# Optimization experiments

Hardware: AMD Instinct MI355X
Metric: run time of the kernel (lower is better)

The kernel has to match this reference:

```python
import jax, jax.numpy as jnp
import numpy as np

B, D_IN, H, D_OUT = 4096, 4096, 2048, 1000
LN_EPS = 1e-5


def setup_inputs() -> dict:
    key = jax.random.key(0)
    ks = jax.random.split(key, 8)
    s_in = 1.0 / np.sqrt(H)  # torch RNN init: U(-1/sqrt(H), 1/sqrt(H))
    inp = {
        "x": jax.random.normal(ks[0], (B, D_IN), dtype=jnp.float32),
        "W_ih0": jax.random.uniform(ks[1], (H, D_IN), jnp.float32, -s_in, s_in),
        "b_ih0": jax.random.uniform(ks[2], (H,), jnp.float32, -s_in, s_in),
        "b_hh0": jax.random.uniform(ks[3], (H,), jnp.float32, -s_in, s_in),
        "W_ih1": jax.random.uniform(ks[4], (H, H), jnp.float32, -s_in, s_in),
        "b_ih1": jax.random.uniform(ks[5], (H,), jnp.float32, -s_in, s_in),
        "b_hh1": jax.random.uniform(ks[6], (H,), jnp.float32, -s_in, s_in),
        "ln_g": jnp.ones((2 * H,), jnp.float32),
        "ln_b": jnp.zeros((2 * H,), jnp.float32),
        "fc_W": jax.random.uniform(ks[7], (D_OUT, 2 * H), jnp.float32, -1.0 / np.sqrt(2 * H), 1.0 / np.sqrt(2 * H)),
        "fc_b": jnp.zeros((D_OUT,), jnp.float32),
    }
    return inp


def reference(x, W_ih0, b_ih0, b_hh0, W_ih1, b_ih1, b_hh1, ln_g, ln_b, fc_W, fc_b):
    # seq_len == 1, h0 == 0 -> W_hh terms vanish; only biases remain.
    h1 = jnp.tanh(x @ W_ih0.T + b_ih0 + b_hh0)          # [B, H]
    h2 = jnp.tanh(h1 @ W_ih1.T + b_ih1 + b_hh1)         # [B, H]
    # last_hidden == mean_pooled (single step) -> concat duplicates h2
    combined = jnp.concatenate([h2, h2], axis=1)        # [B, 2H]
    mu = combined.mean(axis=-1, keepdims=True)
    var = combined.var(axis=-1, keepdims=True)
    normed = (combined - mu) * jax.lax.rsqrt(var + LN_EPS) * ln_g + ln_b
    # dropout is identity in eval mode
    return normed @ fc_W.T + fc_b                        # [B, D_OUT]
```

## Files before the change

kernel.cpp:

```cpp
#include <hip/hip_runtime.h>
#include <hip/hip_bf16.h>

typedef __attribute__((ext_vector_type(8))) unsigned short ushort8;
typedef __attribute__((ext_vector_type(8))) __bf16 bf16x8;
typedef __attribute__((ext_vector_type(4))) float f32x4;
typedef __attribute__((ext_vector_type(4))) float floatx4;

__device__ __forceinline__ unsigned short f2bf(float f) {
    unsigned u = __builtin_bit_cast(unsigned, f);
    u += 0x7fffu + ((u >> 16) & 1u);
    return (unsigned short)(u >> 16);
}
__device__ __forceinline__ float bf2f(unsigned short h) {
    unsigned u = ((unsigned)h) << 16;
    return __builtin_bit_cast(float, u);
}

__device__ __forceinline__ void gload_lds16(const void* g, void* l) {
    __builtin_amdgcn_global_load_lds(
        (const __attribute__((address_space(1))) void*)g,
        (__attribute__((address_space(3))) void*)l,
        16, 0, 0);
}

#define BAR()      asm volatile("s_barrier" ::: "memory")
#define WAIT_VM6() asm volatile("s_waitcnt vmcnt(6)" ::: "memory")
#define WAIT_VM0() asm volatile("s_waitcnt vmcnt(0)" ::: "memory")

__global__ __launch_bounds__(256) void cvt_f2bf(const float* __restrict__ in,
                                                unsigned short* __restrict__ out,
                                                int n8) {
    int i = blockIdx.x * 256 + threadIdx.x;
    if (i >= n8) return;
    floatx4 a = ((const floatx4*)in)[2 * i];
    floatx4 b = ((const floatx4*)in)[2 * i + 1];
    ushort8 o;
#pragma unroll
    for (int j = 0; j < 4; ++j) { o[j] = f2bf(a[j]); o[4 + j] = f2bf(b[j]); }
    ((ushort8*)out)[i] = o;
}

__global__ __launch_bounds__(256) void weff_kernel(const float* __restrict__ fcW,
                                                   const float* __restrict__ lng,
                                                   const float* __restrict__ lnb,
                                                   const float* __restrict__ fcb,
                                                   unsigned short* __restrict__ weff,
                                                   float* __restrict__ cc) {
    int o = blockIdx.x;
    int tid = threadIdx.x;
    if (o >= 1000) {
        ushort8 z = {0, 0, 0, 0, 0, 0, 0, 0};
        ((ushort8*)(weff + (size_t)o * 2048))[tid] = z;
        if (tid == 0) cc[o] = 0.f;
        return;
    }
    const float* wrow = fcW + (size_t)o * 4096;
    int j0 = tid * 8;
    floatx4 wa  = *(const floatx4*)(wrow + j0);
    floatx4 wb  = *(const floatx4*)(wrow + j0 + 4);
    floatx4 wa2 = *(const floatx4*)(wrow + 2048 + j0);
    floatx4 wb2 = *(const floatx4*)(wrow + 2048 + j0 + 4);
    floatx4 ga  = *(const floatx4*)(lng + j0);
    floatx4 gb  = *(const floatx4*)(lng + j0 + 4);
    floatx4 ga2 = *(const floatx4*)(lng + 2048 + j0);
    floatx4 gb2 = *(const floatx4*)(lng + 2048 + j0 + 4);
    floatx4 ba  = *(const floatx4*)(lnb + j0);
    floatx4 bb  = *(const floatx4*)(lnb + j0 + 4);
    floatx4 ba2 = *(const floatx4*)(lnb + 2048 + j0);
    floatx4 bb2 = *(const floatx4*)(lnb + 2048 + j0 + 4);
    ushort8 o8;
    float acc = 0.f;
#pragma unroll
    for (int j = 0; j < 4; ++j) {
        o8[j] = f2bf(ga[j] * wa[j] + ga2[j] * wa2[j]);
        acc += ba[j] * wa[j] + ba2[j] * wa2[j];
        o8[4 + j] = f2bf(gb[j] * wb[j] + gb2[j] * wb2[j]);
        acc += bb[j] * wb[j] + bb2[j] * wb2[j];
    }
    ((ushort8*)(weff + (size_t)o * 2048))[tid] = o8;
#pragma unroll
    for (int d = 32; d; d >>= 1) acc += __shfl_down(acc, d);
    __shared__ float red[4];
    if ((tid & 63) == 0) red[tid >> 6] = acc;
    __syncthreads();
    if (tid == 0) cc[o] = fcb[o] + red[0] + red[1] + red[2] + red[3];
}

__global__ __launch_bounds__(256) void ln_kernel(const unsigned short* __restrict__ h2,
                                                 unsigned short* __restrict__ z) {
    int row = blockIdx.x, tid = threadIdx.x;
    ushort8 v = ((const ushort8*)(h2 + (size_t)row * 2048))[tid];
    float f[8];
    float s = 0.f, s2 = 0.f;
#pragma unroll
    for (int j = 0; j < 8; ++j) { f[j] = bf2f(v[j]); s += f[j]; s2 += f[j] * f[j]; }
#pragma unroll
    for (int d = 32; d; d >>= 1) { s += __shfl_down(s, d); s2 += __shfl_down(s2, d); }
    __shared__ float rs_[4], rs2_[4];
    if ((tid & 63) == 0) { rs_[tid >> 6] = s; rs2_[tid >> 6] = s2; }
    __syncthreads();
    float S = rs_[0] + rs_[1] + rs_[2] + rs_[3];
    float S2 = rs2_[0] + rs2_[1] + rs2_[2] + rs2_[3];
    float mu = S * (1.f / 2048.f);
    float var = S2 * (1.f / 2048.f) - mu * mu;
    float r = rsqrtf(var + 1e-5f);
    ushort8 o;
#pragma unroll
    for (int j = 0; j < 8; ++j) o[j] = f2bf((f[j] - mu) * r);
    ((ushort8*)(z + (size_t)row * 2048))[tid] = o;
}

template <int EPI>
__global__ __launch_bounds__(512, 2) void gemm8p(const unsigned short* __restrict__ A,
                                                 const unsigned short* __restrict__ B,
                                                 int M, int N, int K,
                                                 const float* __restrict__ bias0,
                                                 const float* __restrict__ bias1,
                                                 void* __restrict__ Cout, int ncols) {
    extern __shared__ char smem[];
    const int tid = threadIdx.x;
    const int lane = tid & 63, wid = tid >> 6;
    const int wm = wid >> 2, wn = wid & 3;
    const int fr = lane & 15, g = lane >> 4;

    const int nwg = gridDim.x * gridDim.y;
    const int fid = blockIdx.y * gridDim.x + blockIdx.x;
    const int cpx = nwg >> 3;
    const int sw = (fid & 7) * cpx + (fid >> 3);
    const int bx = sw % gridDim.x, by = sw / gridDim.x;
    const int row0 = by * 128, col0 = bx * 256;

    const int tg = tid >> 3;
    const int tcE = ((tid & 7) ^ (tg & 7)) * 8;

    auto stageA = [&](int kt, char* buf) {
#pragma unroll
        for (int r = 0; r < 2; ++r)
            gload_lds16(A + (size_t)(row0 + r * 64 + tg) * K + kt * 64 + tcE,
                        buf + r * 8192 + wid * 1024);
    };
    auto stageBh = [&](int kt, char* buf, int h) {
#pragma unroll
        for (int r = 0; r < 2; ++r) {
            int rr = h * 2 + r;
            gload_lds16(B + (size_t)(col0 + rr * 64 + tg) * K + kt * 64 + tcE,
                        buf + 16384 + rr * 8192 + wid * 1024);
        }
    };

    const int xorv = (fr & 7) << 4;
    auto rdA = [&](const char* buf, int m, int kh) -> bf16x8 {
        int byte = (wm * 64 + m * 16 + fr) * 128 + ((kh * 64 + g * 16) ^ xorv);
        return __builtin_bit_cast(bf16x8, *(const ushort8*)(buf + byte));
    };
    auto rdB = [&](const char* buf, int n, int kh) -> bf16x8 {
        int byte = 16384 + (wn * 64 + n * 16 + fr) * 128 + ((kh * 64 + g * 16) ^ xorv);
        return __builtin_bit_cast(bf16x8, *(const ushort8*)(buf + byte));
    };

    f32x4 acc[4][4];
#pragma unroll
    for (int i = 0; i < 4; ++i)
#pragma unroll
        for (int j = 0; j < 4; ++j) acc[i][j] = f32x4{0.f, 0.f, 0.f, 0.f};

    char* b0 = smem;
    char* b1 = smem + 49152;
    stageA(0, b0); stageBh(0, b0, 0); stageBh(0, b0, 1);
    stageA(1, b1); stageBh(1, b1, 0); stageBh(1, b1, 1);
    WAIT_VM6();
    BAR();

    const int NT = K >> 6;
    bf16x8 aF[4][2], bF[2][2];
    for (int t = 0; t < NT; ++t) {
        char* rb = smem + (t % 3) * 49152;
        char* wb = smem + ((t + 2) % 3) * 49152;
        const bool st = (t + 2) < NT;

#pragma unroll
        for (int j = 0; j < 2; ++j)
#pragma unroll
            for (int kh = 0; kh < 2; ++kh) bF[j][kh] = rdB(rb, j, kh);
#pragma unroll
        for (int m = 0; m < 4; ++m)
#pragma unroll
            for (int kh = 0; kh < 2; ++kh) aF[m][kh] = rdA(rb, m, kh);
        if (st) { stageA(t + 2, wb); stageBh(t + 2, wb, 0); }
        BAR();
        __builtin_amdgcn_s_setprio(1);
#pragma unroll
        for (int m = 0; m < 4; ++m)
#pragma unroll
            for (int j = 0; j < 2; ++j)
#pragma unroll
                for (int kh = 0; kh < 2; ++kh)
                    acc[m][j] = __builtin_amdgcn_mfma_f32_16x16x32_bf16(aF[m][kh], bF[j][kh], acc[m][j], 0, 0, 0);
        __builtin_amdgcn_s_setprio(0);
        BAR();

#pragma unroll
        for (int j = 0; j < 2; ++j)
#pragma unroll
            for (int kh = 0; kh < 2; ++kh) bF[j][kh] = rdB(rb, 2 + j, kh);
        if (st) stageBh(t + 2, wb, 1);
        BAR();
        __builtin_amdgcn_s_setprio(1);
#pragma unroll
        for (int m = 0; m < 4; ++m)
#pragma unroll
            for (int j = 0; j < 2; ++j)
#pragma unroll
                for (int kh = 0; kh < 2; ++kh)
                    acc[m][2 + j] = __builtin_amdgcn_mfma_f32_16x16x32_bf16(aF[m][kh], bF[j][kh], acc[m][2 + j], 0, 0, 0);
        __builtin_amdgcn_s_setprio(0);
        if (st) { WAIT_VM6(); }
        else if (t + 1 < NT) { WAIT_VM0(); }
        BAR();
    }

#pragma unroll
    for (int i = 0; i < 4; ++i) {
        int rbase = row0 + wm * 64 + i * 16 + g * 4;
#pragma unroll
        for (int j = 0; j < 4; ++j) {
            int col = col0 + wn * 64 + j * 16 + fr;
            if (EPI == 0) {
                float bsum = bias0[col] + bias1[col];
                unsigned short* O = (unsigned short*)Cout;
#pragma unroll
                for (int r = 0; r < 4; ++r)
                    O[(size_t)(rbase + r) * N + col] = f2bf(tanhf(acc[i][j][r] + bsum));
            } else {
                if (col < ncols) {
                    float bsum = bias0[col];
                    float* O = (float*)Cout;
#pragma unroll
                    for (int r = 0; r < 4; ++r)
                        O[(size_t)(rbase + r) * ncols + col] = acc[i][j][r] + bsum;
                }
            }
        }
    }
}

extern "C" void kernel_launch(void* const* d_in, const int* in_sizes, int n_in,
                              void* d_out, int out_size, void* d_ws, size_t ws_size,
                              hipStream_t stream) {
    const float* x   = (const float*)d_in[0];
    const float* W0  = (const float*)d_in[1];
    const float* bi0 = (const float*)d_in[2];
    const float* bh0 = (const float*)d_in[3];
    const float* W1  = (const float*)d_in[4];
    const float* bi1 = (const float*)d_in[5];
    const float* bh1 = (const float*)d_in[6];
    const float* lng = (const float*)d_in[7];
    const float* lnb = (const float*)d_in[8];
    const float* fcW = (const float*)d_in[9];
    const float* fcb = (const float*)d_in[10];
    float* out = (float*)d_out;

    char* w = (char*)d_ws;
    unsigned short* xb   = (unsigned short*)(w);
    unsigned short* w0b  = (unsigned short*)(w + 33554432ull);
    unsigned short* w1b  = (unsigned short*)(w + 50331648ull);
    unsigned short* h1   = (unsigned short*)(w + 58720256ull);
    unsigned short* h2   = (unsigned short*)(w + 75497472ull);
    unsigned short* zb   = (unsigned short*)(w + 92274688ull);
    unsigned short* weff = (unsigned short*)(w + 109051904ull);
    float* cc            = (float*)(w + 113246208ull);

    const int SHM = 147456;
    (void)hipFuncSetAttribute((const void*)gemm8p<0>,
                              hipFuncAttributeMaxDynamicSharedMemorySize, SHM);
    (void)hipFuncSetAttribute((const void*)gemm8p<1>,
                              hipFuncAttributeMaxDynamicSharedMemorySize, SHM);

    cvt_f2bf<<<8192, 256, 0, stream>>>(x,  xb,  2097152);
    cvt_f2bf<<<4096, 256, 0, stream>>>(W0, w0b, 1048576);
    cvt_f2bf<<<2048, 256, 0, stream>>>(W1, w1b, 524288);
    weff_kernel<<<1024, 256, 0, stream>>>(fcW, lng, lnb, fcb, weff, cc);
    gemm8p<0><<<dim3(8, 32), 512, SHM, stream>>>(xb, w0b, 4096, 2048, 4096, bi0, bh0, h1, 2048);
    gemm8p<0><<<dim3(8, 32), 512, SHM, stream>>>(h1, w1b, 4096, 2048, 2048, bi1, bh1, h2, 2048);
    ln_kernel<<<4096, 256, 0, stream>>>(h2, zb);
    gemm8p<1><<<dim3(4, 32), 512, SHM, stream>>>(zb, weff, 4096, 1024, 2048, cc, nullptr, out, 1000);
}
```

Before: 197.3 us.

## Restructure GEMM main loop to one barrier per k-tile with rotating buffers

```diff
diff --git a/kernel.cpp b/kernel.cpp
--- a/kernel.cpp
+++ b/kernel.cpp
@@ -24,8 +24,6 @@
 }
 
 #define BAR()      asm volatile("s_barrier" ::: "memory")
-#define WAIT_VM6() asm volatile("s_waitcnt vmcnt(6)" ::: "memory")
-#define WAIT_VM0() asm volatile("s_waitcnt vmcnt(0)" ::: "memory")
 
 __global__ __launch_bounds__(256) void cvt_f2bf(const float* __restrict__ in,
                                                 unsigned short* __restrict__ out,
@@ -110,14 +108,15 @@
     ((ushort8*)(z + (size_t)row * 2048))[tid] = o;
 }
 
-template <int EPI>
-__global__ __launch_bounds__(512, 2) void gemm8p(const unsigned short* __restrict__ A,
-                                                 const unsigned short* __restrict__ B,
-                                                 int M, int N, int K,
-                                                 const float* __restrict__ bias0,
-                                                 const float* __restrict__ bias1,
-                                                 void* __restrict__ Cout, int ncols) {
+template <int EPI, int NJ>
+__global__ __launch_bounds__(512, 2) void gemm_fr(const unsigned short* __restrict__ A,
+                                                  const unsigned short* __restrict__ B,
+                                                  int M, int N, int K,
+                                                  const float* __restrict__ bias0,
+                                                  const float* __restrict__ bias1,
+                                                  void* __restrict__ Cout, int ncols) {
     extern __shared__ char smem[];
+    constexpr int BUFSZ = 16384 + NJ * 8192;
     const int tid = threadIdx.x;
     const int lane = tid & 63, wid = tid >> 6;
     const int wm = wid >> 2, wn = wid & 3;
@@ -128,7 +127,7 @@
     const int cpx = nwg >> 3;
     const int sw = (fid & 7) * cpx + (fid >> 3);
     const int bx = sw % gridDim.x, by = sw / gridDim.x;
-    const int row0 = by * 128, col0 = bx * 256;
+    const int row0 = by * 128, col0 = bx * (64 * NJ);
 
     const int tg = tid >> 3;
     const int tcE = ((tid & 7) ^ (tg & 7)) * 8;
@@ -139,13 +138,11 @@
             gload_lds16(A + (size_t)(row0 + r * 64 + tg) * K + kt * 64 + tcE,
                         buf + r * 8192 + wid * 1024);
     };
-    auto stageBh = [&](int kt, char* buf, int h) {
-#pragma unroll
-        for (int r = 0; r < 2; ++r) {
-            int rr = h * 2 + r;
+    auto stageB = [&](int kt, char* buf) {
+#pragma unroll
+        for (int rr = 0; rr < NJ; ++rr)
             gload_lds16(B + (size_t)(col0 + rr * 64 + tg) * K + kt * 64 + tcE,
                         buf + 16384 + rr * 8192 + wid * 1024);
-        }
     };
 
     const int xorv = (fr & 7) << 4;
@@ -154,77 +151,64 @@
         return __builtin_bit_cast(bf16x8, *(const ushort8*)(buf + byte));
     };
     auto rdB = [&](const char* buf, int n, int kh) -> bf16x8 {
-        int byte = 16384 + (wn * 64 + n * 16 + fr) * 128 + ((kh * 64 + g * 16) ^ xorv);
+        int byte = 16384 + (wn * (16 * NJ) + n * 16 + fr) * 128 + ((kh * 64 + g * 16) ^ xorv);
         return __builtin_bit_cast(bf16x8, *(const ushort8*)(buf + byte));
     };
 
-    f32x4 acc[4][4];
+    f32x4 acc[4][NJ];
 #pragma unroll
     for (int i = 0; i < 4; ++i)
 #pragma unroll
-        for (int j = 0; j < 4; ++j) acc[i][j] = f32x4{0.f, 0.f, 0.f, 0.f};
-
-    char* b0 = smem;
-    char* b1 = smem + 49152;
-    stageA(0, b0); stageBh(0, b0, 0); stageBh(0, b0, 1);
-    stageA(1, b1); stageBh(1, b1, 0); stageBh(1, b1, 1);
-    WAIT_VM6();
-    BAR();
+        for (int j = 0; j < NJ; ++j) acc[i][j] = f32x4{0.f, 0.f, 0.f, 0.f};
+
+    char* p0 = smem;
+    char* p1 = smem + BUFSZ;
+    char* p2 = smem + 2 * BUFSZ;
+    stageA(0, p0); stageB(0, p0);
+    stageA(1, p1); stageB(1, p1);
 
     const int NT = K >> 6;
-    bf16x8 aF[4][2], bF[2][2];
     for (int t = 0; t < NT; ++t) {
-        char* rb = smem + (t % 3) * 49152;
-        char* wb = smem + ((t + 2) % 3) * 49152;
-        const bool st = (t + 2) < NT;
-
-#pragma unroll
-        for (int j = 0; j < 2; ++j)
-#pragma unroll
-            for (int kh = 0; kh < 2; ++kh) bF[j][kh] = rdB(rb, j, kh);
+        char* rb = p0;
+        char* wb = p2;
+        if (t < NT - 1) {
+            if constexpr (NJ == 4) asm volatile("s_waitcnt vmcnt(6)" ::: "memory");
+            else                   asm volatile("s_waitcnt vmcnt(4)" ::: "memory");
+        } else {
+            asm volatile("s_waitcnt vmcnt(0)" ::: "memory");
+        }
+        BAR();
+        if (t + 2 < NT) { stageA(t + 2, wb); stageB(t + 2, wb); }
+
+        bf16x8 aF[4][2], bF[NJ][2];
 #pragma unroll
         for (int m = 0; m < 4; ++m)
 #pragma unroll
             for (int kh = 0; kh < 2; ++kh) aF[m][kh] = rdA(rb, m, kh);
-        if (st) { stageA(t + 2, wb); stageBh(t + 2, wb, 0); }
-        BAR();
+#pragma unroll
+        for (int n = 0; n < NJ; ++n)
+#pragma unroll
+            for (int kh = 0; kh < 2; ++kh) bF[n][kh] = rdB(rb, n, kh);
+
         __builtin_amdgcn_s_setprio(1);
 #pragma unroll
         for (int m = 0; m < 4; ++m)
 #pragma unroll
-            for (int j = 0; j < 2; ++j)
+            for (int n = 0; n < NJ; ++n)
 #pragma unroll
                 for (int kh = 0; kh < 2; ++kh)
-                    acc[m][j] = __builtin_amdgcn_mfma_f32_16x16x32_bf16(aF[m][kh], bF[j][kh], acc[m][j], 0, 0, 0);
+                    acc[m][n] = __builtin_amdgcn_mfma_f32_16x16x32_bf16(aF[m][kh], bF[n][kh], acc[m][n], 0, 0, 0);
         __builtin_amdgcn_s_setprio(0);
-        BAR();
-
-#pragma unroll
-        for (int j = 0; j < 2; ++j)
-#pragma unroll
-            for (int kh = 0; kh < 2; ++kh) bF[j][kh] = rdB(rb, 2 + j, kh);
-        if (st) stageBh(t + 2, wb, 1);
-        BAR();
-        __builtin_amdgcn_s_setprio(1);
-#pragma unroll
-        for (int m = 0; m < 4; ++m)
-#pragma unroll
-            for (int j = 0; j < 2; ++j)
-#pragma unroll
-                for (int kh = 0; kh < 2; ++kh)
-                    acc[m][2 + j] = __builtin_amdgcn_mfma_f32_16x16x32_bf16(aF[m][kh], bF[j][kh], acc[m][2 + j], 0, 0, 0);
-        __builtin_amdgcn_s_setprio(0);
-        if (st) { WAIT_VM6(); }
-        else if (t + 1 < NT) { WAIT_VM0(); }
-        BAR();
+
+        char* tmp = p0; p0 = p1; p1 = p2; p2 = tmp;
     }
 
 #pragma unroll
     for (int i = 0; i < 4; ++i) {
         int rbase = row0 + wm * 64 + i * 16 + g * 4;
 #pragma unroll
-        for (int j = 0; j < 4; ++j) {
-            int col = col0 + wn * 64 + j * 16 + fr;
+        for (int j = 0; j < NJ; ++j) {
+            int col = col0 + wn * (16 * NJ) + j * 16 + fr;
             if (EPI == 0) {
                 float bsum = bias0[col] + bias1[col];
                 unsigned short* O = (unsigned short*)Cout;
@@ -270,18 +254,19 @@
     unsigned short* weff = (unsigned short*)(w + 109051904ull);
     float* cc            = (float*)(w + 113246208ull);
 
-    const int SHM = 147456;
-    (void)hipFuncSetAttribute((const void*)gemm8p<0>,
-                              hipFuncAttributeMaxDynamicSharedMemorySize, SHM);
-    (void)hipFuncSetAttribute((const void*)gemm8p<1>,
-                              hipFuncAttributeMaxDynamicSharedMemorySize, SHM);
+    const int SHM0 = 3 * (16384 + 4 * 8192);
+    const int SHM1 = 3 * (16384 + 2 * 8192);
+    (void)hipFuncSetAttribute((const void*)gemm_fr<0, 4>,
+                              hipFuncAttributeMaxDynamicSharedMemorySize, SHM0);
+    (void)hipFuncSetAttribute((const void*)gemm_fr<1, 2>,
+                              hipFuncAttributeMaxDynamicSharedMemorySize, SHM1);
 
     cvt_f2bf<<<8192, 256, 0, stream>>>(x,  xb,  2097152);
     cvt_f2bf<<<4096, 256, 0, stream>>>(W0, w0b, 1048576);
     cvt_f2bf<<<2048, 256, 0, stream>>>(W1, w1b, 524288);
     weff_kernel<<<1024, 256, 0, stream>>>(fcW, lng, lnb, fcb, weff, cc);
-    gemm8p<0><<<dim3(8, 32), 512, SHM, stream>>>(xb, w0b, 4096, 2048, 4096, bi0, bh0, h1, 2048);
-    gemm8p<0><<<dim3(8, 32), 512, SHM, stream>>>(h1, w1b, 4096, 2048, 2048, bi1, bh1, h2, 2048);
+    gemm_fr<0, 4><<<dim3(8, 32), 512, SHM0, stream>>>(xb, w0b, 4096, 2048, 4096, bi0, bh0, h1, 2048);
+    gemm_fr<0, 4><<<dim3(8, 32), 512, SHM0, stream>>>(h1, w1b, 4096, 2048, 2048, bi1, bh1, h2, 2048);
     ln_kernel<<<4096, 256, 0, stream>>>(h2, zb);
-    gemm8p<1><<<dim3(4, 32), 512, SHM, stream>>>(zb, weff, 4096, 1024, 2048, cc, nullptr, out, 1000);
-}
+    gemm_fr<1, 2><<<dim3(8, 32), 512, SHM1, stream>>>(zb, weff, 4096, 1024, 2048, cc, nullptr, out, 1000);
+}
```

Result: faster. 174.2 us (-11.7%).
